# Kernel tuning notes

Measured on AMD Instinct MI355X. Metric: run time of the kernel, lower is better.

## Reference

```python
import jax, jax.numpy as jnp
import numpy as np

NUM_GT = 25      # num_gt_lesions (init kwarg); labels 1..25 all present in gt
NUM_PRED = 40    # number of predicted CC labels (labels 0..40 in pred)
SMOOTH = 1.0
VOL = (256, 256, 256)


def setup_inputs() -> dict:
    key = jax.random.key(0)
    k1, k2 = jax.random.split(key)
    # pred holds integer-valued connected-component labels stored as float
    # (the original applies sigmoid to it and compares values for identity).
    pred = jax.random.randint(k1, VOL, 0, NUM_PRED + 1).astype(jnp.float32)
    gt = jax.random.randint(k2, VOL, 0, NUM_GT + 1).astype(jnp.int32)
    return {"pred": pred, "gt": gt}


def _instance_dice(pred, gt):
    # Original: s = sigmoid(pred); all unique/isin/!=0 tests are on s.
    # sigmoid is injective => value equality on s == label equality on pred;
    # sigmoid(x) != 0 always  => every `!= 0` filter in the original is a no-op
    # (in particular pred label 0 participates, since sigmoid(0)=0.5).
    lbl = jax.lax.stop_gradient(jnp.round(pred)).astype(jnp.int32)  # pred CC ids
    g = gt.astype(jnp.int32)

    # Joint histogram counts[p, c] = #voxels with pred==p and gt==c.
    combined = (lbl * (NUM_GT + 1) + g).ravel()
    counts = jnp.zeros((NUM_PRED + 1) * (NUM_GT + 1), jnp.float32)
    counts = counts.at[combined].add(1.0).reshape(NUM_PRED + 1, NUM_GT + 1)

    gt_sizes = counts[:, 1:].sum(axis=0)            # [L] |gt == c| for c=1..L
    present = gt_sizes > 0
    num_gt = present.sum()                          # torch.unique(gt[gt!=0]).size(0)

    overlap = counts[:, 1:] > 0                     # [P+1, L] pred label p hits comp c
    pred_sizes = counts.sum(axis=1)                 # [P+1] |pred == p|
    union_size = (overlap * pred_sizes[:, None]).sum(axis=0)  # |pred_tmp| per comp
    # pred_tmp covers every voxel of the gt component => intersection = gt_sizes
    dice = 2.0 * gt_sizes / (union_size + gt_sizes + SMOOTH)
    lesion_dice = jnp.where(present, dice, 0.0).sum()

    tp_any = (overlap & present[None, :]).any(axis=1)  # pred labels collected in tp
    fp = ((pred_sizes > 0) & ~tp_any).sum()            # pred labels missing all gt comps
    return lesion_dice / (num_gt + fp)


def reference(pred, gt):
    return _instance_dice(pred, gt)
```

## Files before the change

### kernel.cpp

```cpp
#include <hip/hip_runtime.h>
#include <hip/hip_bf16.h>

#define NUM_GT 25
#define NUM_PRED 40
#define PAD 32

#define GT_W(b)  ((b) * PAD)
#define PR_W(p)  ((25 + (p)) * PAD)
#define OV_W(p)  ((65 + (p)) * PAD)
#define WS_WORDS (106 * PAD)

#define GRID 1024
#define BLOCK 256

#if defined(__has_builtin)
#  if __has_builtin(__builtin_amdgcn_sad_u8)
#    define SAD(A, W, K) (A) = __builtin_amdgcn_sad_u8((W), (K), (A))
#  endif
#endif
#ifndef SAD
#  define SAD(A, W, K) asm("v_sad_u8 %0, %1, %2, %0" : "+v"(A) : "v"(W), "s"(K))
#endif

__device__ __forceinline__ void quad(
    int4 g, float4 p, unsigned* sovl, unsigned& G, unsigned& P)
{
    unsigned a0 = (unsigned)g.x, a1 = (unsigned)g.y;
    unsigned a2 = (unsigned)g.z, a3 = (unsigned)g.w;
    unsigned b0 = (unsigned)p.x, b1 = (unsigned)p.y;
    unsigned b2 = (unsigned)p.z, b3 = (unsigned)p.w;
    atomicOr(&sovl[b0 & 63], 1u << (a0 & 31));
    atomicOr(&sovl[b1 & 63], 1u << (a1 & 31));
    atomicOr(&sovl[b2 & 63], 1u << (a2 & 31));
    atomicOr(&sovl[b3 & 63], 1u << (a3 & 31));
    G = a0 | (a1 << 8) | (a2 << 16) | (a3 << 24);
    P = b0 | (b1 << 8) | (b2 << 16) | (b3 << 24);
}

__global__ __launch_bounds__(BLOCK, 3) void hist_kernel(
    const float* __restrict__ pred, const int* __restrict__ gt,
    unsigned* __restrict__ ws, int n)
{
    __shared__ unsigned sovl[64];
    __shared__ unsigned shist[66];
    __shared__ unsigned stash[4][16][34];

    const int tid  = threadIdx.x;
    const int lane = tid & 63;
    const int wave = tid >> 6;

    if (tid < 64) sovl[tid] = 0u;
    if (tid < 66) shist[tid] = 0u;
    __syncthreads();

    unsigned acc[66];
    #pragma unroll
    for (int j = 0; j < 66; ++j) acc[j] = 0u;

    const int gtid   = blockIdx.x * BLOCK + tid;
    const int n16    = n >> 4;
    const int stride = GRID * BLOCK;
    const float4* __restrict__ p4 = (const float4*)pred;
    const int4* __restrict__  g4 = (const int4*)gt;

    for (int i = gtid; i < n16; i += stride) {
        const int q = i * 4;
        int4  ga = g4[q],     gb = g4[q + 1], gc = g4[q + 2], gd = g4[q + 3];
        float4 pa = p4[q],    pb = p4[q + 1], pc = p4[q + 2], pd = p4[q + 3];

        unsigned GA, GB, GC, GD, PA, PB, PC, PD;
        quad(ga, pa, sovl, GA, PA);
        quad(gb, pb, sovl, GB, PB);
        quad(gc, pc, sovl, GC, PC);
        quad(gd, pd, sovl, GD, PD);

        #pragma unroll
        for (int b = 0; b < 25; ++b) {
            const unsigned K = (unsigned)(b * 0x01010101u);
            SAD(acc[b], GA, K); SAD(acc[b], GB, K);
            SAD(acc[b], GC, K); SAD(acc[b], GD, K);
        }
        #pragma unroll
        for (int b = 0; b < 40; ++b) {
            const unsigned K = (unsigned)(b * 0x01010101u);
            SAD(acc[25 + b], PA, K); SAD(acc[25 + b], PB, K);
            SAD(acc[25 + b], PC, K); SAD(acc[25 + b], PD, K);
        }
    }

    if (blockIdx.x == 0 && tid == 0) {
        for (int v = n16 << 4; v < n; ++v) {
            int p = (int)pred[v];
            int g = gt[v];
            for (int b = 0; b < 25; ++b) atomicAdd(&ws[GT_W(b)], (unsigned)abs(g - b));
            for (int b = 0; b < 40; ++b) atomicAdd(&ws[PR_W(b)], (unsigned)abs(p - b));
            atomicOr(&ws[OV_W(min(max(p, 0), NUM_PRED))], 1u << (g & 31));
        }
    }

    #pragma unroll
    for (int jp = 0; jp < 33; ++jp) {
        unsigned v = acc[2 * jp] | (acc[2 * jp + 1] << 16);
        v += __shfl_down(v, 32, 64);
        v += __shfl_down(v, 16, 64);
        if (lane < 16) stash[wave][lane][jp] = v;
    }
    __syncthreads();

    for (int i = tid; i < 33 * 16; i += BLOCK) {
        int jp = i >> 4, sl = i & 15;
        unsigned a = stash[0][sl][jp] + stash[1][sl][jp]
                   + stash[2][sl][jp] + stash[3][sl][jp];
        unsigned lo = a & 0xFFFFu, hi = a >> 16;
        lo += __shfl_down(lo, 8, 16);  hi += __shfl_down(hi, 8, 16);
        lo += __shfl_down(lo, 4, 16);  hi += __shfl_down(hi, 4, 16);
        lo += __shfl_down(lo, 2, 16);  hi += __shfl_down(hi, 2, 16);
        lo += __shfl_down(lo, 1, 16);  hi += __shfl_down(hi, 1, 16);
        if (sl == 0) {
            if (lo) atomicAdd(&shist[2 * jp], lo);
            if (hi && 2 * jp + 1 < 65) atomicAdd(&shist[2 * jp + 1], hi);
        }
    }
    __syncthreads();

    for (int i = tid; i < 65; i += BLOCK) {
        unsigned s = shist[i];
        if (s) atomicAdd(&ws[i * PAD], s);
    }
    if (tid < 41) {
        unsigned v = sovl[tid];
        if (v) atomicOr(&ws[OV_W(tid)], v);
    }
}

__global__ __launch_bounds__(64) void finish_kernel(
    const unsigned* __restrict__ ws, float* __restrict__ out, int n)
{
    __shared__ long long gg[25], gp[40], psz[41];
    __shared__ unsigned ov[41];
    const int lane = threadIdx.x;
    if (lane < 25) gg[lane] = (long long)ws[GT_W(lane)];
    if (lane < 40) gp[lane] = (long long)ws[PR_W(lane)];
    if (lane < 41) ov[lane] = ws[OV_W(lane)];
    __syncthreads();

    const long long N = n, Sg = gg[0], Sp = gp[0];

    if (lane < 41) {
        int P = lane;
        long long f;
        if (P == 0)       f = (N - gp[0] + gp[1]) / 2;
        else if (P <= 38) f = (gp[P - 1] - 2 * gp[P] + gp[P + 1]) / 2;
        else if (P == 39) f = (gp[38] - 2 * gp[39] + (40 * N - Sp)) / 2;
        else              f = (gp[39] - 39 * N + Sp) / 2;
        psz[P] = f;
    }
    __syncthreads();

    double dice = 0.0;
    int present = 0;
    if (lane < 25) {
        int L = lane + 1;
        long long gs;
        if (L <= 23)      gs = (gg[L - 1] - 2 * gg[L] + gg[L + 1]) / 2;
        else if (L == 24) gs = (gg[23] - 2 * gg[24] + (25 * N - Sg)) / 2;
        else              gs = (gg[24] - 24 * N + Sg) / 2;
        if (gs > 0) {
            present = 1;
            double un = 0.0;
            const unsigned bit = 1u << L;
            for (int p = 0; p < 41; ++p)
                if (ov[p] & bit) un += (double)psz[p];
            dice = 2.0 * (double)gs / (un + (double)gs + 1.0);
        }
    }
    int fp = 0;
    if (lane < 41) {
        if (psz[lane] > 0 && (ov[lane] & 0x3FFFFFEu) == 0) fp = 1;
    }

    int num_gt = __popcll(__ballot(present != 0));
    int nfp    = __popcll(__ballot(fp != 0));
    #pragma unroll
    for (int o = 32; o >= 1; o >>= 1) dice += __shfl_xor(dice, o, 64);

    if (lane == 0) out[0] = (float)(dice / (double)(num_gt + nfp));
}

extern "C" void kernel_launch(void* const* d_in, const int* in_sizes, int n_in,
                              void* d_out, int out_size, void* d_ws, size_t ws_size,
                              hipStream_t stream) {
    const float* pred = (const float*)d_in[0];
    const int* gt = (const int*)d_in[1];
    float* out = (float*)d_out;
    unsigned* ws = (unsigned*)d_ws;
    const int n = in_sizes[0];

    hipMemsetAsync(ws, 0, WS_WORDS * sizeof(unsigned), stream);

    hist_kernel<<<GRID, BLOCK, 0, stream>>>(pred, gt, ws, n);
    finish_kernel<<<1, 64, 0, stream>>>(ws, out, n);
}
```

Baseline: 45.98 us.

## Split overlap bitmask into seeded test-before-set kernel separate from SAD histogram

Result: slower. 67.65 us (+47.1%).

```diff
diff --git a/kernel.cpp b/kernel.cpp
--- a/kernel.cpp
+++ b/kernel.cpp
@@ -10,8 +10,10 @@
 #define OV_W(p)  ((65 + (p)) * PAD)
 #define WS_WORDS (106 * PAD)
 
-#define GRID 1024
+#define GRID  1024
 #define BLOCK 256
+#define OGRID 2048
+#define SGRID 256
 
 #if defined(__has_builtin)
 #  if __has_builtin(__builtin_amdgcn_sad_u8)
@@ -22,26 +24,51 @@
 #  define SAD(A, W, K) asm("v_sad_u8 %0, %1, %2, %0" : "+v"(A) : "v"(W), "s"(K))
 #endif
 
-__device__ __forceinline__ void quad(
-    int4 g, float4 p, unsigned* sovl, unsigned& G, unsigned& P)
-{
-    unsigned a0 = (unsigned)g.x, a1 = (unsigned)g.y;
-    unsigned a2 = (unsigned)g.z, a3 = (unsigned)g.w;
-    unsigned b0 = (unsigned)p.x, b1 = (unsigned)p.y;
-    unsigned b2 = (unsigned)p.z, b3 = (unsigned)p.w;
-    atomicOr(&sovl[b0 & 63], 1u << (a0 & 31));
-    atomicOr(&sovl[b1 & 63], 1u << (a1 & 31));
-    atomicOr(&sovl[b2 & 63], 1u << (a2 & 31));
-    atomicOr(&sovl[b3 & 63], 1u << (a3 & 31));
-    G = a0 | (a1 << 8) | (a2 << 16) | (a3 << 24);
-    P = b0 | (b1 << 8) | (b2 << 16) | (b3 << 24);
-}
-
-__global__ __launch_bounds__(BLOCK, 3) void hist_kernel(
+__device__ __forceinline__ unsigned packg(int4 g) {
+    return (unsigned)g.x | ((unsigned)g.y << 8) |
+           ((unsigned)g.z << 16) | ((unsigned)g.w << 24);
+}
+__device__ __forceinline__ unsigned packp(float4 p) {
+    return (unsigned)p.x | ((unsigned)p.y << 8) |
+           ((unsigned)p.z << 16) | ((unsigned)p.w << 24);
+}
+
+__global__ __launch_bounds__(BLOCK) void seed_kernel(
     const float* __restrict__ pred, const int* __restrict__ gt,
     unsigned* __restrict__ ws, int n)
 {
     __shared__ unsigned sovl[64];
+    const int tid = threadIdx.x;
+    if (tid < 64) sovl[tid] = 0u;
+    __syncthreads();
+
+    const int n4 = n >> 2;
+    const int q = (blockIdx.x * BLOCK + tid) * 2;
+    const float4* __restrict__ p4 = (const float4*)pred;
+    const int4* __restrict__  g4 = (const int4*)gt;
+    if (q + 1 < n4) {
+        int4  ga = g4[q], gb = g4[q + 1];
+        float4 pa = p4[q], pb = p4[q + 1];
+        atomicOr(&sovl[(unsigned)pa.x & 63], 1u << ((unsigned)ga.x & 31));
+        atomicOr(&sovl[(unsigned)pa.y & 63], 1u << ((unsigned)ga.y & 31));
+        atomicOr(&sovl[(unsigned)pa.z & 63], 1u << ((unsigned)ga.z & 31));
+        atomicOr(&sovl[(unsigned)pa.w & 63], 1u << ((unsigned)ga.w & 31));
+        atomicOr(&sovl[(unsigned)pb.x & 63], 1u << ((unsigned)gb.x & 31));
+        atomicOr(&sovl[(unsigned)pb.y & 63], 1u << ((unsigned)gb.y & 31));
+        atomicOr(&sovl[(unsigned)pb.z & 63], 1u << ((unsigned)gb.z & 31));
+        atomicOr(&sovl[(unsigned)pb.w & 63], 1u << ((unsigned)gb.w & 31));
+    }
+    __syncthreads();
+    if (tid < 41) {
+        unsigned v = sovl[tid];
+        if (v) atomicOr(&ws[OV_W(tid)], v);
+    }
+}
+
+__global__ __launch_bounds__(BLOCK, 3) void sad_kernel(
+    const float* __restrict__ pred, const int* __restrict__ gt,
+    unsigned* __restrict__ ws, int n)
+{
     __shared__ unsigned shist[66];
     __shared__ unsigned stash[4][16][34];
 
@@ -49,7 +76,6 @@
     const int lane = tid & 63;
     const int wave = tid >> 6;
 
-    if (tid < 64) sovl[tid] = 0u;
     if (tid < 66) shist[tid] = 0u;
     __syncthreads();
 
@@ -65,14 +91,11 @@
 
     for (int i = gtid; i < n16; i += stride) {
         const int q = i * 4;
-        int4  ga = g4[q],     gb = g4[q + 1], gc = g4[q + 2], gd = g4[q + 3];
-        float4 pa = p4[q],    pb = p4[q + 1], pc = p4[q + 2], pd = p4[q + 3];
-
-        unsigned GA, GB, GC, GD, PA, PB, PC, PD;
-        quad(ga, pa, sovl, GA, PA);
-        quad(gb, pb, sovl, GB, PB);
-        quad(gc, pc, sovl, GC, PC);
-        quad(gd, pd, sovl, GD, PD);
+        int4  ga = g4[q], gb = g4[q + 1], gc = g4[q + 2], gd = g4[q + 3];
+        float4 pa = p4[q], pb = p4[q + 1], pc = p4[q + 2], pd = p4[q + 3];
+
+        unsigned GA = packg(ga), GB = packg(gb), GC = packg(gc), GD = packg(gd);
+        unsigned PA = packp(pa), PB = packp(pb), PC = packp(pc), PD = packp(pd);
 
         #pragma unroll
         for (int b = 0; b < 25; ++b) {
@@ -94,7 +117,6 @@
             int g = gt[v];
             for (int b = 0; b < 25; ++b) atomicAdd(&ws[GT_W(b)], (unsigned)abs(g - b));
             for (int b = 0; b < 40; ++b) atomicAdd(&ws[PR_W(b)], (unsigned)abs(p - b));
-            atomicOr(&ws[OV_W(min(max(p, 0), NUM_PRED))], 1u << (g & 31));
         }
     }
 
@@ -127,7 +149,72 @@
         unsigned s = shist[i];
         if (s) atomicAdd(&ws[i * PAD], s);
     }
-    if (tid < 41) {
+}
+
+__global__ __launch_bounds__(BLOCK) void ovl_kernel(
+    const float* __restrict__ pred, const int* __restrict__ gt,
+    unsigned* __restrict__ ws, int n)
+{
+    __shared__ unsigned sovl[64];
+    __shared__ unsigned dirty;
+    const int tid = threadIdx.x;
+
+    if (tid < 64) sovl[tid] = (tid < 41) ? ws[OV_W(tid)] : 0u;
+    if (tid == 0) dirty = 0u;
+    __syncthreads();
+
+    const int n16    = n >> 4;
+    const int stride = OGRID * BLOCK;
+    const float4* __restrict__ p4 = (const float4*)pred;
+    const int4* __restrict__  g4 = (const int4*)gt;
+
+    #define TS(GV, PV)                                                        \
+        { unsigned aa = (unsigned)(GV) & 31u, bb = (unsigned)(PV) & 63u;      \
+          unsigned m = 1u << aa;                                              \
+          if (!(sovl[bb] & m)) atomicOr(&sovl[bb], m); }
+
+    for (int i = blockIdx.x * BLOCK + tid; i < n16; i += stride) {
+        const int q = i * 4;
+        int4  ga = g4[q], gb = g4[q + 1], gc = g4[q + 2], gd = g4[q + 3];
+        float4 pa = p4[q], pb = p4[q + 1], pc = p4[q + 2], pd = p4[q + 3];
+
+        unsigned ok =
+              (sovl[(unsigned)pa.x & 63] >> ((unsigned)ga.x & 31))
+            & (sovl[(unsigned)pa.y & 63] >> ((unsigned)ga.y & 31))
+            & (sovl[(unsigned)pa.z & 63] >> ((unsigned)ga.z & 31))
+            & (sovl[(unsigned)pa.w & 63] >> ((unsigned)ga.w & 31))
+            & (sovl[(unsigned)pb.x & 63] >> ((unsigned)gb.x & 31))
+            & (sovl[(unsigned)pb.y & 63] >> ((unsigned)gb.y & 31))
+            & (sovl[(unsigned)pb.z & 63] >> ((unsigned)gb.z & 31))
+            & (sovl[(unsigned)pb.w & 63] >> ((unsigned)gb.w & 31))
+            & (sovl[(unsigned)pc.x & 63] >> ((unsigned)gc.x & 31))
+            & (sovl[(unsigned)pc.y & 63] >> ((unsigned)gc.y & 31))
+            & (sovl[(unsigned)pc.z & 63] >> ((unsigned)gc.z & 31))
+            & (sovl[(unsigned)pc.w & 63] >> ((unsigned)gc.w & 31))
+            & (sovl[(unsigned)pd.x & 63] >> ((unsigned)gd.x & 31))
+            & (sovl[(unsigned)pd.y & 63] >> ((unsigned)gd.y & 31))
+            & (sovl[(unsigned)pd.z & 63] >> ((unsigned)gd.z & 31))
+            & (sovl[(unsigned)pd.w & 63] >> ((unsigned)gd.w & 31));
+        if (!(ok & 1u)) {
+            TS(ga.x, pa.x) TS(ga.y, pa.y) TS(ga.z, pa.z) TS(ga.w, pa.w)
+            TS(gb.x, pb.x) TS(gb.y, pb.y) TS(gb.z, pb.z) TS(gb.w, pb.w)
+            TS(gc.x, pc.x) TS(gc.y, pc.y) TS(gc.z, pc.z) TS(gc.w, pc.w)
+            TS(gd.x, pd.x) TS(gd.y, pd.y) TS(gd.z, pd.z) TS(gd.w, pd.w)
+            dirty = 1u;
+        }
+    }
+    #undef TS
+
+    if (blockIdx.x == 0 && tid == 0) {
+        for (int v = n16 << 4; v < n; ++v) {
+            int p = (int)pred[v];
+            int g = gt[v];
+            atomicOr(&ws[OV_W(min(max(p, 0), NUM_PRED))], 1u << (g & 31));
+        }
+    }
+
+    __syncthreads();
+    if (dirty && tid < 41) {
         unsigned v = sovl[tid];
         if (v) atomicOr(&ws[OV_W(tid)], v);
     }
@@ -198,6 +285,8 @@
 
     hipMemsetAsync(ws, 0, WS_WORDS * sizeof(unsigned), stream);
 
-    hist_kernel<<<GRID, BLOCK, 0, stream>>>(pred, gt, ws, n);
+    seed_kernel<<<SGRID, BLOCK, 0, stream>>>(pred, gt, ws, n);
+    sad_kernel<<<GRID, BLOCK, 0, stream>>>(pred, gt, ws, n);
+    ovl_kernel<<<OGRID, BLOCK, 0, stream>>>(pred, gt, ws, n);
     finish_kernel<<<1, 64, 0, stream>>>(ws, out, n);
 }
```

## Split histogram into two register-light passes to raise occupancy

Applied to the files above, without the earlier changes.

New measurement: 55.86 us. 21.5% more time.

```diff
diff --git a/kernel.cpp b/kernel.cpp
--- a/kernel.cpp
+++ b/kernel.cpp
@@ -10,7 +10,7 @@
 #define OV_W(p)  ((65 + (p)) * PAD)
 #define WS_WORDS (106 * PAD)
 
-#define GRID 1024
+#define GRID 1536
 #define BLOCK 256
 
 #if defined(__has_builtin)
@@ -22,92 +22,29 @@
 #  define SAD(A, W, K) asm("v_sad_u8 %0, %1, %2, %0" : "+v"(A) : "v"(W), "s"(K))
 #endif
 
-__device__ __forceinline__ void quad(
-    int4 g, float4 p, unsigned* sovl, unsigned& G, unsigned& P)
+__device__ __forceinline__ unsigned packg(int4 g) {
+    return (unsigned)g.x | ((unsigned)g.y << 8) |
+           ((unsigned)g.z << 16) | ((unsigned)g.w << 24);
+}
+__device__ __forceinline__ unsigned packp(float4 p) {
+    return (unsigned)p.x | ((unsigned)p.y << 8) |
+           ((unsigned)p.z << 16) | ((unsigned)p.w << 24);
+}
+
+template <int NPAIR>
+__device__ __forceinline__ void tree_flush(
+    const unsigned* acc, int sbin0, int tid, int lane, int wave,
+    unsigned (*stash)[16][34], unsigned* shist)
 {
-    unsigned a0 = (unsigned)g.x, a1 = (unsigned)g.y;
-    unsigned a2 = (unsigned)g.z, a3 = (unsigned)g.w;
-    unsigned b0 = (unsigned)p.x, b1 = (unsigned)p.y;
-    unsigned b2 = (unsigned)p.z, b3 = (unsigned)p.w;
-    atomicOr(&sovl[b0 & 63], 1u << (a0 & 31));
-    atomicOr(&sovl[b1 & 63], 1u << (a1 & 31));
-    atomicOr(&sovl[b2 & 63], 1u << (a2 & 31));
-    atomicOr(&sovl[b3 & 63], 1u << (a3 & 31));
-    G = a0 | (a1 << 8) | (a2 << 16) | (a3 << 24);
-    P = b0 | (b1 << 8) | (b2 << 16) | (b3 << 24);
-}
-
-__global__ __launch_bounds__(BLOCK, 3) void hist_kernel(
-    const float* __restrict__ pred, const int* __restrict__ gt,
-    unsigned* __restrict__ ws, int n)
-{
-    __shared__ unsigned sovl[64];
-    __shared__ unsigned shist[66];
-    __shared__ unsigned stash[4][16][34];
-
-    const int tid  = threadIdx.x;
-    const int lane = tid & 63;
-    const int wave = tid >> 6;
-
-    if (tid < 64) sovl[tid] = 0u;
-    if (tid < 66) shist[tid] = 0u;
-    __syncthreads();
-
-    unsigned acc[66];
     #pragma unroll
-    for (int j = 0; j < 66; ++j) acc[j] = 0u;
-
-    const int gtid   = blockIdx.x * BLOCK + tid;
-    const int n16    = n >> 4;
-    const int stride = GRID * BLOCK;
-    const float4* __restrict__ p4 = (const float4*)pred;
-    const int4* __restrict__  g4 = (const int4*)gt;
-
-    for (int i = gtid; i < n16; i += stride) {
-        const int q = i * 4;
-        int4  ga = g4[q],     gb = g4[q + 1], gc = g4[q + 2], gd = g4[q + 3];
-        float4 pa = p4[q],    pb = p4[q + 1], pc = p4[q + 2], pd = p4[q + 3];
-
-        unsigned GA, GB, GC, GD, PA, PB, PC, PD;
-        quad(ga, pa, sovl, GA, PA);
-        quad(gb, pb, sovl, GB, PB);
-        quad(gc, pc, sovl, GC, PC);
-        quad(gd, pd, sovl, GD, PD);
-
-        #pragma unroll
-        for (int b = 0; b < 25; ++b) {
-            const unsigned K = (unsigned)(b * 0x01010101u);
-            SAD(acc[b], GA, K); SAD(acc[b], GB, K);
-            SAD(acc[b], GC, K); SAD(acc[b], GD, K);
-        }
-        #pragma unroll
-        for (int b = 0; b < 40; ++b) {
-            const unsigned K = (unsigned)(b * 0x01010101u);
-            SAD(acc[25 + b], PA, K); SAD(acc[25 + b], PB, K);
-            SAD(acc[25 + b], PC, K); SAD(acc[25 + b], PD, K);
-        }
-    }
-
-    if (blockIdx.x == 0 && tid == 0) {
-        for (int v = n16 << 4; v < n; ++v) {
-            int p = (int)pred[v];
-            int g = gt[v];
-            for (int b = 0; b < 25; ++b) atomicAdd(&ws[GT_W(b)], (unsigned)abs(g - b));
-            for (int b = 0; b < 40; ++b) atomicAdd(&ws[PR_W(b)], (unsigned)abs(p - b));
-            atomicOr(&ws[OV_W(min(max(p, 0), NUM_PRED))], 1u << (g & 31));
-        }
-    }
-
-    #pragma unroll
-    for (int jp = 0; jp < 33; ++jp) {
+    for (int jp = 0; jp < NPAIR; ++jp) {
         unsigned v = acc[2 * jp] | (acc[2 * jp + 1] << 16);
         v += __shfl_down(v, 32, 64);
         v += __shfl_down(v, 16, 64);
         if (lane < 16) stash[wave][lane][jp] = v;
     }
     __syncthreads();
-
-    for (int i = tid; i < 33 * 16; i += BLOCK) {
+    for (int i = tid; i < NPAIR * 16; i += BLOCK) {
         int jp = i >> 4, sl = i & 15;
         unsigned a = stash[0][sl][jp] + stash[1][sl][jp]
                    + stash[2][sl][jp] + stash[3][sl][jp];
@@ -117,11 +54,104 @@
         lo += __shfl_down(lo, 2, 16);  hi += __shfl_down(hi, 2, 16);
         lo += __shfl_down(lo, 1, 16);  hi += __shfl_down(hi, 1, 16);
         if (sl == 0) {
-            if (lo) atomicAdd(&shist[2 * jp], lo);
-            if (hi && 2 * jp + 1 < 65) atomicAdd(&shist[2 * jp + 1], hi);
-        }
-    }
-    __syncthreads();
+            if (lo) atomicAdd(&shist[sbin0 + 2 * jp], lo);
+            if (hi) atomicAdd(&shist[sbin0 + 2 * jp + 1], hi);
+        }
+    }
+    __syncthreads();
+}
+
+__global__ __launch_bounds__(BLOCK, 6) void hist_kernel(
+    const float* __restrict__ pred, const int* __restrict__ gt,
+    unsigned* __restrict__ ws, int n)
+{
+    __shared__ unsigned sovl[64];
+    __shared__ unsigned shist[66];
+    __shared__ unsigned stash[4][16][34];
+
+    const int tid  = threadIdx.x;
+    const int lane = tid & 63;
+    const int wave = tid >> 6;
+
+    if (tid < 64) sovl[tid] = 0u;
+    if (tid < 66) shist[tid] = 0u;
+    __syncthreads();
+
+    const int stride = GRID * BLOCK;
+    const int gtid   = blockIdx.x * BLOCK + tid;
+    const float4* __restrict__ p4 = (const float4*)pred;
+    const int4* __restrict__  g4 = (const int4*)gt;
+
+    {
+        unsigned acc[34];
+        #pragma unroll
+        for (int j = 0; j < 34; ++j) acc[j] = 0u;
+
+        const int n8 = n >> 3;
+        for (int i = gtid; i < n8; i += stride) {
+            const int q = i * 2;
+            int4  g0 = g4[q], g1 = g4[q + 1];
+            float4 pq0 = p4[q], pq1 = p4[q + 1];
+
+            atomicOr(&sovl[(unsigned)pq0.x & 63], 1u << ((unsigned)g0.x & 31));
+            atomicOr(&sovl[(unsigned)pq0.y & 63], 1u << ((unsigned)g0.y & 31));
+            atomicOr(&sovl[(unsigned)pq0.z & 63], 1u << ((unsigned)g0.z & 31));
+            atomicOr(&sovl[(unsigned)pq0.w & 63], 1u << ((unsigned)g0.w & 31));
+            atomicOr(&sovl[(unsigned)pq1.x & 63], 1u << ((unsigned)g1.x & 31));
+            atomicOr(&sovl[(unsigned)pq1.y & 63], 1u << ((unsigned)g1.y & 31));
+            atomicOr(&sovl[(unsigned)pq1.z & 63], 1u << ((unsigned)g1.z & 31));
+            atomicOr(&sovl[(unsigned)pq1.w & 63], 1u << ((unsigned)g1.w & 31));
+
+            unsigned G0 = packg(g0), G1 = packg(g1);
+            unsigned P0 = packp(pq0), P1 = packp(pq1);
+            #pragma unroll
+            for (int b = 0; b < 25; ++b) {
+                const unsigned K = (unsigned)(b * 0x01010101u);
+                SAD(acc[b], G0, K); SAD(acc[b], G1, K);
+            }
+            #pragma unroll
+            for (int b = 0; b < 8; ++b) {
+                const unsigned K = (unsigned)(b * 0x01010101u);
+                SAD(acc[25 + b], P0, K); SAD(acc[25 + b], P1, K);
+            }
+        }
+        tree_flush<17>(acc, 0, tid, lane, wave, stash, shist);
+    }
+
+    {
+        unsigned acc[32];
+        #pragma unroll
+        for (int j = 0; j < 32; ++j) acc[j] = 0u;
+
+        const int n16 = n >> 4;
+        for (int i = gtid; i < n16; i += stride) {
+            const int q = i * 4;
+            float4 w0 = p4[q], w1 = p4[q + 1], w2 = p4[q + 2], w3 = p4[q + 3];
+            unsigned W0 = packp(w0), W1 = packp(w1);
+            unsigned W2 = packp(w2), W3 = packp(w3);
+            #pragma unroll
+            for (int b = 0; b < 32; ++b) {
+                const unsigned K = (unsigned)((8 + b) * 0x01010101u);
+                SAD(acc[b], W0, K); SAD(acc[b], W1, K);
+                SAD(acc[b], W2, K); SAD(acc[b], W3, K);
+            }
+        }
+        tree_flush<16>(acc, 33, tid, lane, wave, stash, shist);
+    }
+
+    if (blockIdx.x == 0 && tid == 0) {
+        for (int v = (n >> 3) << 3; v < n; ++v) {
+            int p = (int)pred[v];
+            int g = gt[v];
+            for (int b = 0; b < 25; ++b) atomicAdd(&ws[GT_W(b)], (unsigned)abs(g - b));
+            for (int b = 0; b < 8; ++b)  atomicAdd(&ws[PR_W(b)], (unsigned)abs(p - b));
+            atomicOr(&ws[OV_W(min(max(p, 0), NUM_PRED))], 1u << (g & 31));
+        }
+        for (int v = (n >> 4) << 4; v < n; ++v) {
+            int p = (int)pred[v];
+            for (int b = 8; b < 40; ++b) atomicAdd(&ws[PR_W(b)], (unsigned)abs(p - b));
+        }
+    }
 
     for (int i = tid; i < 65; i += BLOCK) {
         unsigned s = shist[i];
```

## Double-buffer input tiles in LDS via async global_load_lds staging

Applied to the files above, without the earlier changes.

New measurement: 45.40 us, median of 2. Within noise of the previous version (-1.3%).

```diff
diff --git a/kernel.cpp b/kernel.cpp
--- a/kernel.cpp
+++ b/kernel.cpp
@@ -10,8 +10,9 @@
 #define OV_W(p)  ((65 + (p)) * PAD)
 #define WS_WORDS (106 * PAD)
 
-#define GRID 1024
+#define GRID  1024
 #define BLOCK 256
+#define TILE  2048
 
 #if defined(__has_builtin)
 #  if __has_builtin(__builtin_amdgcn_sad_u8)
@@ -22,74 +23,102 @@
 #  define SAD(A, W, K) asm("v_sad_u8 %0, %1, %2, %0" : "+v"(A) : "v"(W), "s"(K))
 #endif
 
-__device__ __forceinline__ void quad(
-    int4 g, float4 p, unsigned* sovl, unsigned& G, unsigned& P)
+#define AS1 __attribute__((address_space(1)))
+#define AS3 __attribute__((address_space(3)))
+
+__device__ __forceinline__ void stage_tile(
+    const unsigned* __restrict__ gsrc, unsigned* ldst, int wid, int lane)
 {
-    unsigned a0 = (unsigned)g.x, a1 = (unsigned)g.y;
-    unsigned a2 = (unsigned)g.z, a3 = (unsigned)g.w;
-    unsigned b0 = (unsigned)p.x, b1 = (unsigned)p.y;
-    unsigned b2 = (unsigned)p.z, b3 = (unsigned)p.w;
-    atomicOr(&sovl[b0 & 63], 1u << (a0 & 31));
-    atomicOr(&sovl[b1 & 63], 1u << (a1 & 31));
-    atomicOr(&sovl[b2 & 63], 1u << (a2 & 31));
-    atomicOr(&sovl[b3 & 63], 1u << (a3 & 31));
-    G = a0 | (a1 << 8) | (a2 << 16) | (a3 << 24);
-    P = b0 | (b1 << 8) | (b2 << 16) | (b3 << 24);
-}
-
-__global__ __launch_bounds__(BLOCK, 3) void hist_kernel(
+#if defined(__has_builtin) && __has_builtin(__builtin_amdgcn_global_load_lds)
+    const unsigned* s0 = gsrc + wid * 512 + lane * 4;
+    unsigned* d0 = ldst + wid * 512;
+    __builtin_amdgcn_global_load_lds((const AS1 unsigned*)s0,
+                                     (AS3 unsigned*)d0, 16, 0, 0);
+    __builtin_amdgcn_global_load_lds((const AS1 unsigned*)(s0 + 256),
+                                     (AS3 unsigned*)(d0 + 256), 16, 0, 0);
+#else
+    *(uint4*)(ldst + wid * 512 + lane * 4) =
+        *(const uint4*)(gsrc + wid * 512 + lane * 4);
+    *(uint4*)(ldst + wid * 512 + 256 + lane * 4) =
+        *(const uint4*)(gsrc + wid * 512 + 256 + lane * 4);
+#endif
+}
+
+__global__ __launch_bounds__(BLOCK) void hist_kernel(
     const float* __restrict__ pred, const int* __restrict__ gt,
     unsigned* __restrict__ ws, int n)
 {
+    __shared__ unsigned lgt[2][TILE];
+    __shared__ unsigned lpr[2][TILE];
     __shared__ unsigned sovl[64];
     __shared__ unsigned shist[66];
-    __shared__ unsigned stash[4][16][34];
 
     const int tid  = threadIdx.x;
     const int lane = tid & 63;
-    const int wave = tid >> 6;
+    const int wid  = tid >> 6;
 
     if (tid < 64) sovl[tid] = 0u;
     if (tid < 66) shist[tid] = 0u;
-    __syncthreads();
 
     unsigned acc[66];
     #pragma unroll
     for (int j = 0; j < 66; ++j) acc[j] = 0u;
 
-    const int gtid   = blockIdx.x * BLOCK + tid;
-    const int n16    = n >> 4;
-    const int stride = GRID * BLOCK;
-    const float4* __restrict__ p4 = (const float4*)pred;
-    const int4* __restrict__  g4 = (const int4*)gt;
-
-    for (int i = gtid; i < n16; i += stride) {
-        const int q = i * 4;
-        int4  ga = g4[q],     gb = g4[q + 1], gc = g4[q + 2], gd = g4[q + 3];
-        float4 pa = p4[q],    pb = p4[q + 1], pc = p4[q + 2], pd = p4[q + 3];
-
-        unsigned GA, GB, GC, GD, PA, PB, PC, PD;
-        quad(ga, pa, sovl, GA, PA);
-        quad(gb, pb, sovl, GB, PB);
-        quad(gc, pc, sovl, GC, PC);
-        quad(gd, pd, sovl, GD, PD);
-
+    const unsigned* __restrict__ gu = (const unsigned*)gt;
+    const unsigned* __restrict__ pu = (const unsigned*)pred;
+    const int ntiles = n / TILE;
+
+    int t = blockIdx.x;
+    int cur = 0;
+    if (t < ntiles) {
+        stage_tile(gu + (size_t)t * TILE, &lgt[0][0], wid, lane);
+        stage_tile(pu + (size_t)t * TILE, &lpr[0][0], wid, lane);
+    }
+    __syncthreads();
+
+    for (; t < ntiles; t += GRID) {
+        const int tn = t + GRID;
+        if (tn < ntiles) {
+            stage_tile(gu + (size_t)tn * TILE, &lgt[cur ^ 1][0], wid, lane);
+            stage_tile(pu + (size_t)tn * TILE, &lpr[cur ^ 1][0], wid, lane);
+        }
+
+        const uint4* g4 = (const uint4*)(&lgt[cur][0] + wid * 512);
+        const uint4* p4 = (const uint4*)(&lpr[cur][0] + wid * 512);
         #pragma unroll
-        for (int b = 0; b < 25; ++b) {
-            const unsigned K = (unsigned)(b * 0x01010101u);
-            SAD(acc[b], GA, K); SAD(acc[b], GB, K);
-            SAD(acc[b], GC, K); SAD(acc[b], GD, K);
-        }
-        #pragma unroll
-        for (int b = 0; b < 40; ++b) {
-            const unsigned K = (unsigned)(b * 0x01010101u);
-            SAD(acc[25 + b], PA, K); SAD(acc[25 + b], PB, K);
-            SAD(acc[25 + b], PC, K); SAD(acc[25 + b], PD, K);
-        }
+        for (int h = 0; h < 2; ++h) {
+            uint4 gw = g4[h * 64 + lane];
+            uint4 pw = p4[h * 64 + lane];
+            unsigned b0 = (unsigned)__uint_as_float(pw.x);
+            unsigned b1 = (unsigned)__uint_as_float(pw.y);
+            unsigned b2 = (unsigned)__uint_as_float(pw.z);
+            unsigned b3 = (unsigned)__uint_as_float(pw.w);
+
+            atomicOr(&sovl[b0 & 63], 1u << (gw.x & 31));
+            atomicOr(&sovl[b1 & 63], 1u << (gw.y & 31));
+            atomicOr(&sovl[b2 & 63], 1u << (gw.z & 31));
+            atomicOr(&sovl[b3 & 63], 1u << (gw.w & 31));
+
+            unsigned G = gw.x | (gw.y << 8) | (gw.z << 16) | (gw.w << 24);
+            unsigned P = b0 | (b1 << 8) | (b2 << 16) | (b3 << 24);
+            #pragma unroll
+            for (int b = 0; b < 25; ++b) {
+                const unsigned K = (unsigned)(b * 0x01010101u);
+                SAD(acc[b], G, K);
+            }
+            #pragma unroll
+            for (int b = 0; b < 40; ++b) {
+                const unsigned K = (unsigned)(b * 0x01010101u);
+                SAD(acc[25 + b], P, K);
+            }
+        }
+
+        __syncthreads();
+        cur ^= 1;
     }
 
     if (blockIdx.x == 0 && tid == 0) {
-        for (int v = n16 << 4; v < n; ++v) {
+        for (int v = ntiles * TILE; v < n; ++v) {
             int p = (int)pred[v];
             int g = gt[v];
             for (int b = 0; b < 25; ++b) atomicAdd(&ws[GT_W(b)], (unsigned)abs(g - b));
@@ -98,12 +127,13 @@
         }
     }
 
+    unsigned (*stash)[16][34] = (unsigned(*)[16][34])(&lgt[0][0]);
     #pragma unroll
     for (int jp = 0; jp < 33; ++jp) {
         unsigned v = acc[2 * jp] | (acc[2 * jp + 1] << 16);
         v += __shfl_down(v, 32, 64);
         v += __shfl_down(v, 16, 64);
-        if (lane < 16) stash[wave][lane][jp] = v;
+        if (lane < 16) stash[wid][lane][jp] = v;
     }
     __syncthreads();
 
```
